# Performance work log

Measured on AMD Instinct MI355X. Metric: run time of the kernel, lower is better.

Reference implementation:

```python
import jax, jax.numpy as jnp
import numpy as np

N = 50000              # total nodes
E = 800000             # random edges (self loops added inside reference, as PyG GATConv does)
FD = 3                 # feature_dim_node
C = 64                 # hidden_channels (= out after heads=1 concat)
OUT = 64               # out_channels of conv2
FC = 512               # fc_hidden_dim
NODES_PER_GRAPH = 5000
NUM_GRAPHS = N // NODES_PER_GRAPH
NEG_SLOPE = 0.2        # PyG GATConv default negative_slope


def _gat(x, W, a_s, a_d, b, src, dst):
    """Single-head PyG GATConv: gather -> leaky_relu -> segment softmax over dst -> scatter-sum."""
    n = x.shape[0]
    h = x @ W                       # [N, C]
    e_s = h @ a_s                   # [N] alpha contribution of source nodes
    e_d = h @ a_d                   # [N] alpha contribution of dest nodes
    e = e_s[src] + e_d[dst]         # [E+N] per-edge logits
    e = jnp.where(e > 0, e, NEG_SLOPE * e)  # leaky_relu
    m = jax.ops.segment_max(e, dst, num_segments=n)
    p = jnp.exp(e - m[dst])
    s = jax.ops.segment_sum(p, dst, num_segments=n)
    alpha = p / s[dst]              # segment softmax over incoming edges of each dst
    out = jax.ops.segment_sum(alpha[:, None] * h[src], dst, num_segments=n)
    return out + b


def setup_inputs() -> dict:
    key = jax.random.key(0)
    ks = jax.random.split(key, 20)
    p = lambda k, shape: (jax.random.normal(k, shape, jnp.float32) * 0.1)
    inp = {
        "x": jax.random.normal(ks[0], (N, FD), jnp.float32),
        "edge_index": jax.random.randint(ks[1], (2, E), 0, N, jnp.int64),
        # conv1: FD -> C
        "W1": p(ks[2], (FD, C)), "as1": p(ks[3], (C,)), "ad1": p(ks[4], (C,)), "b1": p(ks[5], (C,)),
        # 2 hidden convs: C -> C (num_layers - 2 = 2)
        "Wh": p(ks[6], (2, C, C)), "ash": p(ks[7], (2, C)), "adh": p(ks[8], (2, C)), "bh": p(ks[9], (2, C)),
        # conv2: C -> OUT
        "W2": p(ks[10], (C, OUT)), "as2": p(ks[11], (OUT,)), "ad2": p(ks[12], (OUT,)), "b2": p(ks[13], (OUT,)),
        # value head MLP
        "Wv1": p(ks[14], (OUT, FC)), "bv1": p(ks[15], (FC,)),
        "Wv2": p(ks[16], (FC, 1)), "bv2": p(ks[17], (1,)),
    }
    return inp


def reference(x, edge_index, W1, as1, ad1, b1, Wh, ash, adh, bh,
              W2, as2, ad2, b2, Wv1, bv1, Wv2, bv2):
    loops = jnp.arange(N, dtype=edge_index.dtype)
    src = jnp.concatenate([edge_index[0], loops])   # add self loops (PyG default)
    dst = jnp.concatenate([edge_index[1], loops])

    h = jax.nn.relu(_gat(x, W1, as1, ad1, b1, src, dst))
    for i in range(2):  # fixed small layer loop
        h = jax.nn.relu(_gat(h, Wh[i], ash[i], adh[i], bh[i], src, dst))
    h = _gat(h, W2, as2, ad2, b2, src, dst)          # [N, OUT] node embeddings (no relu)

    batch = jnp.arange(N) // NODES_PER_GRAPH          # create_batch_tensor
    pooled = jax.ops.segment_sum(h, batch, num_segments=NUM_GRAPHS) / NODES_PER_GRAPH
    value = jax.nn.relu(pooled @ Wv1 + bv1) @ Wv2 + bv2   # [NUM_GRAPHS, 1]
    return h, pooled, value
```

## Files before the change

kernel.cpp:

```cpp
#include <hip/hip_runtime.h>
#include <hip/hip_fp16.h>
#include <math.h>

#define NN 50000
#define EE 800000
#define TOT_EDGES (EE + NN)
#define FD 3
#define C 64
#define FC 512
#define NODES_PER_GRAPH 5000
#define NUM_GRAPHS 10
#define POOL_CHUNKS 40
#define POOL_NODES_PER_CHUNK 125
#define NEG_SLOPE 0.2f

#define SCAN_BLK 1024
#define SCAN_GRID ((NN + SCAN_BLK - 1) / SCAN_BLK)

#define HC_BLOCKS 1024

#define NPART 8
#define PART_NODES ((NN + NPART - 1) / NPART)
#define CSR_EPT 8
#define CSR_CHUNK (256 * CSR_EPT)
#define CSR_CHUNKS ((TOT_EDGES + CSR_CHUNK - 1) / CSR_CHUNK)


__global__ void k_init_counts(int* counts) {
    int i = blockIdx.x * blockDim.x + threadIdx.x;
    if (i < NN) counts[i] = 0;
}

__global__ void k_count_part(const int* __restrict__ dst, int* __restrict__ counts) {
    int part = blockIdx.x & (NPART - 1);
    int chunk = blockIdx.x >> 3;
    int lo = part * PART_NODES, hi = lo + PART_NODES;
    int base = chunk * CSR_CHUNK + threadIdx.x;
#pragma unroll
    for (int e = 0; e < CSR_EPT; ++e) {
        int i = base + e * 256;
        if (i < TOT_EDGES) {
            int d = (i < EE) ? dst[i] : (i - EE);
            if (d >= lo && d < hi) atomicAdd(&counts[d], 1);
        }
    }
}

__global__ void k_scan1(const int* __restrict__ counts, int* __restrict__ offsets,
                        int* __restrict__ blocksums) {
    int tid = threadIdx.x, blk = blockIdx.x;
    int i = blk * SCAN_BLK + tid;
    int v = (i < NN) ? counts[i] : 0;
    __shared__ int buf[SCAN_BLK];
    buf[tid] = v;
    __syncthreads();
    for (int off = 1; off < SCAN_BLK; off <<= 1) {
        int t = (tid >= off) ? buf[tid - off] : 0;
        __syncthreads();
        buf[tid] += t;
        __syncthreads();
    }
    if (i < NN) offsets[i] = buf[tid] - v;
    if (tid == SCAN_BLK - 1) blocksums[blk] = buf[tid];
}

__global__ void k_scan2(int* __restrict__ blocksums, int* __restrict__ offsets) {
    if (threadIdx.x == 0) {
        int run = 0;
        for (int b = 0; b < SCAN_GRID; ++b) {
            int v = blocksums[b];
            blocksums[b] = run;
            run += v;
        }
        offsets[NN] = run;
    }
}

__global__ void k_scan3(int* __restrict__ offsets, int* __restrict__ cursors,
                        const int* __restrict__ blocksums) {
    int tid = threadIdx.x, blk = blockIdx.x;
    int i = blk * SCAN_BLK + tid;
    if (i < NN) {
        int o = offsets[i] + blocksums[blk];
        offsets[i] = o;
        cursors[i] = o;
    }
}

__global__ void k_scatter_part(const int* __restrict__ src, const int* __restrict__ dst,
                               int* __restrict__ cursors, int* __restrict__ ssrc) {
    int part = blockIdx.x & (NPART - 1);
    int chunk = blockIdx.x >> 3;
    int lo = part * PART_NODES, hi = lo + PART_NODES;
    int base = chunk * CSR_CHUNK + threadIdx.x;
#pragma unroll
    for (int e = 0; e < CSR_EPT; ++e) {
        int i = base + e * 256;
        if (i < TOT_EDGES) {
            int d = (i < EE) ? dst[i] : (i - EE);
            if (d >= lo && d < hi) {
                int s = (i < EE) ? src[i] : d;
                int idx = atomicAdd(&cursors[d], 1);
                ssrc[idx] = s;
            }
        }
    }
}


__global__ void k_hcompute_f3(const float* __restrict__ x,
                              const float* __restrict__ W,
                              const float* __restrict__ a_s, const float* __restrict__ a_d,
                              __half* __restrict__ h, float* __restrict__ es,
                              float* __restrict__ ed, int nwaves_total) {
    int lane = threadIdx.x & 63;
    int wid = (blockIdx.x * blockDim.x + threadIdx.x) >> 6;

    float wcol[FD];
#pragma unroll
    for (int k = 0; k < FD; ++k) wcol[k] = W[k * 64 + lane];
    float asl = a_s[lane], adl = a_d[lane];

    for (int n = wid; n < NN; n += nwaves_total) {
        int nu = __builtin_amdgcn_readfirstlane(n);
        const float* xrow = x + (size_t)nu * FD;
        float acc = 0.f;
#pragma unroll
        for (int k = 0; k < FD; ++k) acc = fmaf(xrow[k], wcol[k], acc);
        h[(size_t)nu * 64 + lane] = __float2half(acc);
        float vs = acc * asl;
        float vd = acc * adl;
        for (int w = 32; w >= 1; w >>= 1) {
            vs += __shfl_xor(vs, w);
            vd += __shfl_xor(vd, w);
        }
        if (lane == 0) { es[nu] = vs; ed[nu] = vd; }
    }
}

__global__ void k_hcompute_h64(const __half* __restrict__ x,
                               const float* __restrict__ W,
                               const float* __restrict__ a_s, const float* __restrict__ a_d,
                               __half* __restrict__ h, float* __restrict__ es,
                               float* __restrict__ ed, int nwaves_total) {
    int lane = threadIdx.x & 63;
    int wid = (blockIdx.x * blockDim.x + threadIdx.x) >> 6;

    float wcol[64];
#pragma unroll
    for (int k = 0; k < 64; ++k) wcol[k] = W[k * 64 + lane];
    float asl = a_s[lane], adl = a_d[lane];

    for (int n = wid; n < NN; n += nwaves_total) {
        int nu = __builtin_amdgcn_readfirstlane(n);
        const __half2* xr = (const __half2*)(x + (size_t)nu * 64);
        float acc = 0.f;
#pragma unroll
        for (int q = 0; q < 32; ++q) {
            float2 f = __half22float2(xr[q]);
            acc = fmaf(f.x, wcol[2 * q], acc);
            acc = fmaf(f.y, wcol[2 * q + 1], acc);
        }
        h[(size_t)nu * 64 + lane] = __float2half(acc);
        float vs = acc * asl;
        float vd = acc * adl;
        for (int w = 32; w >= 1; w >>= 1) {
            vs += __shfl_xor(vs, w);
            vd += __shfl_xor(vd, w);
        }
        if (lane == 0) { es[nu] = vs; ed[nu] = vd; }
    }
}

template<int HIDDEN>
__global__ void k_aggregate(const __half* __restrict__ h,
                            const float* __restrict__ es, const float* __restrict__ ed,
                            const int* __restrict__ offsets, const int* __restrict__ ssrc,
                            const float* __restrict__ bias,
                            __half* __restrict__ outH, float* __restrict__ outF) {
    int gtid = blockIdx.x * blockDim.x + threadIdx.x;
    int n = gtid >> 6;
    int lane = threadIdx.x & 63;
    if (n >= NN) return;
    int beg = offsets[n], end = offsets[n + 1];
    float ednv = ed[n];

    int grp = lane >> 3;
    int c   = lane & 7;
    float s = 0.f;
    float acc[8];
#pragma unroll
    for (int i = 0; i < 8; ++i) acc[i] = 0.f;

    for (int j0 = beg; j0 < end; j0 += 16) {
        int jg0 = j0 + grp;
        int jg1 = j0 + 8 + grp;
        bool v0 = jg0 < end, v1 = jg1 < end;
        int sj0 = v0 ? ssrc[jg0] : 0;
        int sj1 = v1 ? ssrc[jg1] : 0;
        float4 raw0 = *(const float4*)&h[(size_t)sj0 * 64 + c * 8];
        float4 raw1 = *(const float4*)&h[(size_t)sj1 * 64 + c * 8];
        float e0 = es[sj0] + ednv;
        float e1 = es[sj1] + ednv;
        e0 = (e0 > 0.f) ? e0 : NEG_SLOPE * e0;
        e1 = (e1 > 0.f) ? e1 : NEG_SLOPE * e1;
        float p0 = v0 ? __expf(e0) : 0.f;
        float p1 = v1 ? __expf(e1) : 0.f;
        s += p0;
        const __half2* hp0 = (const __half2*)&raw0;
#pragma unroll
        for (int q = 0; q < 4; ++q) {
            float2 f = __half22float2(hp0[q]);
            acc[2 * q]     = fmaf(p0, f.x, acc[2 * q]);
            acc[2 * q + 1] = fmaf(p0, f.y, acc[2 * q + 1]);
        }
        s += p1;
        const __half2* hp1 = (const __half2*)&raw1;
#pragma unroll
        for (int q = 0; q < 4; ++q) {
            float2 f = __half22float2(hp1[q]);
            acc[2 * q]     = fmaf(p1, f.x, acc[2 * q]);
            acc[2 * q + 1] = fmaf(p1, f.y, acc[2 * q + 1]);
        }
    }
#pragma unroll
    for (int w = 8; w <= 32; w <<= 1) {
        s += __shfl_xor(s, w);
#pragma unroll
        for (int i = 0; i < 8; ++i) acc[i] += __shfl_xor(acc[i], w);
    }
    if (grp == 0) {
        float inv_s = 1.0f / s;
        float v[8];
#pragma unroll
        for (int i = 0; i < 8; ++i) {
            v[i] = acc[i] * inv_s + bias[c * 8 + i];
            if (HIDDEN) v[i] = fmaxf(v[i], 0.f);
        }
        if (HIDDEN) {
            __half2 hv[4];
#pragma unroll
            for (int q = 0; q < 4; ++q)
                hv[q] = __floats2half2_rn(v[2 * q], v[2 * q + 1]);
            *(float4*)&outH[(size_t)n * 64 + c * 8] = *(float4*)hv;
        } else {
            *(float4*)&outF[(size_t)n * 64 + c * 8]     = make_float4(v[0], v[1], v[2], v[3]);
            *(float4*)&outF[(size_t)n * 64 + c * 8 + 4] = make_float4(v[4], v[5], v[6], v[7]);
        }
    }
}


__global__ void k_pool1(const float* __restrict__ h, float* __restrict__ partial) {
    int blk = blockIdx.x;
    int g = blk / POOL_CHUNKS, c = blk % POOL_CHUNKS;
    int wave = threadIdx.x >> 6, lane = threadIdx.x & 63;
    int base = g * NODES_PER_GRAPH + c * POOL_NODES_PER_CHUNK;
    float acc = 0.f;
    for (int i = wave; i < POOL_NODES_PER_CHUNK; i += 4)
        acc += h[(size_t)(base + i) * 64 + lane];
    __shared__ float buf[4][64];
    buf[wave][lane] = acc;
    __syncthreads();
    if (wave == 0)
        partial[blk * 64 + lane] = buf[0][lane] + buf[1][lane] + buf[2][lane] + buf[3][lane];
}

__global__ void k_pool2(const float* __restrict__ partial, float* __restrict__ pooled) {
    int g = blockIdx.x;
    int lane = threadIdx.x;
    float acc = 0.f;
    for (int c = 0; c < POOL_CHUNKS; ++c)
        acc += partial[(g * POOL_CHUNKS + c) * 64 + lane];
    pooled[g * 64 + lane] = acc * (1.0f / NODES_PER_GRAPH);
}

__global__ void k_value(const float* __restrict__ pooled,
                        const float* __restrict__ Wv1, const float* __restrict__ bv1,
                        const float* __restrict__ Wv2, const float* __restrict__ bv2,
                        float* __restrict__ value) {
    int g = blockIdx.x;
    int j = threadIdx.x;
    __shared__ float pl[64];
    if (j < 64) pl[j] = pooled[g * 64 + j];
    __syncthreads();
    float acc = bv1[j];
    for (int c = 0; c < 64; ++c) acc += pl[c] * Wv1[c * 512 + j];
    acc = fmaxf(acc, 0.f);
    float t = acc * Wv2[j];
    for (int w = 32; w >= 1; w >>= 1) t += __shfl_xor(t, w);
    __shared__ float red[8];
    int wave = j >> 6, lane = j & 63;
    if (lane == 0) red[wave] = t;
    __syncthreads();
    if (j == 0) {
        float v = 0.f;
        for (int w = 0; w < 8; ++w) v += red[w];
        value[g] = v + bv2[0];
    }
}


extern "C" void kernel_launch(void* const* d_in, const int* in_sizes, int n_in,
                              void* d_out, int out_size, void* d_ws, size_t ws_size,
                              hipStream_t stream) {
    const float* x   = (const float*)d_in[0];
    const int*   ei  = (const int*)d_in[1];
    const float* W1  = (const float*)d_in[2];
    const float* as1 = (const float*)d_in[3];
    const float* ad1 = (const float*)d_in[4];
    const float* b1  = (const float*)d_in[5];
    const float* Wh  = (const float*)d_in[6];
    const float* ash = (const float*)d_in[7];
    const float* adh = (const float*)d_in[8];
    const float* bh  = (const float*)d_in[9];
    const float* W2  = (const float*)d_in[10];
    const float* as2 = (const float*)d_in[11];
    const float* ad2 = (const float*)d_in[12];
    const float* b2  = (const float*)d_in[13];
    const float* Wv1 = (const float*)d_in[14];
    const float* bv1 = (const float*)d_in[15];
    const float* Wv2 = (const float*)d_in[16];
    const float* bv2 = (const float*)d_in[17];

    const int* e_src = ei;
    const int* e_dst = ei + EE;

    char* p = (char*)d_ws;
    auto carve = [&](size_t bytes) {
        char* r = p;
        p += (bytes + 255) & ~(size_t)255;
        return r;
    };
    int*    counts    = (int*)carve(NN * 4);
    int*    offsets   = (int*)carve((NN + 1) * 4);
    int*    cursors   = (int*)carve(NN * 4);
    int*    ssrc      = (int*)carve(TOT_EDGES * 4);
    int*    blocksums = (int*)carve(SCAN_GRID * 4);
    __half* bufH      = (__half*)carve((size_t)NN * 64 * 2);
    __half* bufB16    = (__half*)carve((size_t)NN * 64 * 2);
    float*  es        = (float*)carve(NN * 4);
    float*  ed        = (float*)carve(NN * 4);
    float*  partial   = (float*)carve((size_t)NUM_GRAPHS * POOL_CHUNKS * 64 * 4);

    float* out_h      = (float*)d_out;
    float* out_pooled = out_h + (size_t)NN * 64;
    float* out_value  = out_pooled + NUM_GRAPHS * 64;

    k_init_counts<<<(NN + 255) / 256, 256, 0, stream>>>(counts);
    k_count_part<<<NPART * CSR_CHUNKS, 256, 0, stream>>>(e_dst, counts);
    k_scan1<<<SCAN_GRID, SCAN_BLK, 0, stream>>>(counts, offsets, blocksums);
    k_scan2<<<1, 64, 0, stream>>>(blocksums, offsets);
    k_scan3<<<SCAN_GRID, SCAN_BLK, 0, stream>>>(offsets, cursors, blocksums);
    k_scatter_part<<<NPART * CSR_CHUNKS, 256, 0, stream>>>(e_src, e_dst, cursors, ssrc);

    const int HBLK = (NN + 3) / 4;
    const int HC_WAVES = HC_BLOCKS * 256 / 64;

    k_hcompute_f3<<<HC_BLOCKS, 256, 0, stream>>>(x, W1, as1, ad1, bufH, es, ed, HC_WAVES);
    k_aggregate<1><<<HBLK, 256, 0, stream>>>(bufH, es, ed, offsets, ssrc, b1, bufB16, nullptr);

    for (int i = 0; i < 2; ++i) {
        k_hcompute_h64<<<HC_BLOCKS, 256, 0, stream>>>(bufB16, Wh + i * 64 * 64, ash + i * 64,
                                                      adh + i * 64, bufH, es, ed, HC_WAVES);
        k_aggregate<1><<<HBLK, 256, 0, stream>>>(bufH, es, ed, offsets, ssrc, bh + i * 64,
                                                 bufB16, nullptr);
    }

    k_hcompute_h64<<<HC_BLOCKS, 256, 0, stream>>>(bufB16, W2, as2, ad2, bufH, es, ed, HC_WAVES);
    k_aggregate<0><<<HBLK, 256, 0, stream>>>(bufH, es, ed, offsets, ssrc, b2, nullptr, out_h);

    k_pool1<<<NUM_GRAPHS * POOL_CHUNKS, 256, 0, stream>>>(out_h, partial);
    k_pool2<<<NUM_GRAPHS, 64, 0, stream>>>(partial, out_pooled);
    k_value<<<NUM_GRAPHS, 512, 0, stream>>>(out_pooled, Wv1, bv1, Wv2, bv2, out_value);
}
```

Before: 280.3 us.

## Compute hidden-layer linear transforms with MFMA 16x16x32 f16 instructions

Replaces the per-node scalar FMA dense transform (one wave per node, 64 FMAs per lane) with a matrix-core kernel in which each wave computes a 16-row stripe using mfma_f32_16x16x32_f16. Weights are pre-packed once into fp16 fragment layout by a new small kernel. The attention dot products are reduced with shuffles over the accumulator layout. This cuts ALU work and redundant weight loads in the three 64x64 transforms, at the cost of fp16 weight rounding and one extra launch.

```diff
diff --git a/kernel.cpp b/kernel.cpp
--- a/kernel.cpp
+++ b/kernel.cpp
@@ -19,11 +19,17 @@
 
 #define HC_BLOCKS 1024
 
+#define STRIPES (NN / 16)
+#define MFMA_BLOCKS ((STRIPES + 3) / 4)
+
 #define NPART 8
 #define PART_NODES ((NN + NPART - 1) / NPART)
 #define CSR_EPT 8
 #define CSR_CHUNK (256 * CSR_EPT)
 #define CSR_CHUNKS ((TOT_EDGES + CSR_CHUNK - 1) / CSR_CHUNK)
+
+typedef _Float16 f16x8 __attribute__((ext_vector_type(8)));
+typedef float f32x4 __attribute__((ext_vector_type(4)));
 
 
 __global__ void k_init_counts(int* counts) {
@@ -107,6 +113,20 @@
     }
 }
 
+__global__ void k_wpack(const float* __restrict__ Wh, const float* __restrict__ W2,
+                        __half* __restrict__ wpack) {
+    int tid = blockIdx.x * blockDim.x + threadIdx.x;
+    if (tid >= 3 * 8 * 64) return;
+    int l = tid & 63, f = (tid >> 6) & 7, layer = tid >> 9;
+    const float* W = (layer == 0) ? Wh : (layer == 1) ? (Wh + 4096) : W2;
+    int t = f >> 1, h = f & 1;
+#pragma unroll
+    for (int j = 0; j < 8; ++j) {
+        float w = W[(h * 32 + (l >> 4) * 8 + j) * 64 + (t * 16 + (l & 15))];
+        wpack[(size_t)tid * 8 + j] = __float2half(w);
+    }
+}
+
 
 __global__ void k_hcompute_f3(const float* __restrict__ x,
                               const float* __restrict__ W,
@@ -138,37 +158,61 @@
     }
 }
 
-__global__ void k_hcompute_h64(const __half* __restrict__ x,
-                               const float* __restrict__ W,
-                               const float* __restrict__ a_s, const float* __restrict__ a_d,
-                               __half* __restrict__ h, float* __restrict__ es,
-                               float* __restrict__ ed, int nwaves_total) {
+__global__ void k_hc_mfma(const __half* __restrict__ X,
+                          const __half* __restrict__ wpack,
+                          const float* __restrict__ a_s, const float* __restrict__ a_d,
+                          __half* __restrict__ H, float* __restrict__ es,
+                          float* __restrict__ ed) {
     int lane = threadIdx.x & 63;
-    int wid = (blockIdx.x * blockDim.x + threadIdx.x) >> 6;
-
-    float wcol[64];
-#pragma unroll
-    for (int k = 0; k < 64; ++k) wcol[k] = W[k * 64 + lane];
-    float asl = a_s[lane], adl = a_d[lane];
-
-    for (int n = wid; n < NN; n += nwaves_total) {
-        int nu = __builtin_amdgcn_readfirstlane(n);
-        const __half2* xr = (const __half2*)(x + (size_t)nu * 64);
-        float acc = 0.f;
-#pragma unroll
-        for (int q = 0; q < 32; ++q) {
-            float2 f = __half22float2(xr[q]);
-            acc = fmaf(f.x, wcol[2 * q], acc);
-            acc = fmaf(f.y, wcol[2 * q + 1], acc);
-        }
-        h[(size_t)nu * 64 + lane] = __float2half(acc);
-        float vs = acc * asl;
-        float vd = acc * adl;
-        for (int w = 32; w >= 1; w >>= 1) {
-            vs += __shfl_xor(vs, w);
-            vd += __shfl_xor(vd, w);
-        }
-        if (lane == 0) { es[nu] = vs; ed[nu] = vd; }
+    int stripe = (blockIdx.x * blockDim.x + threadIdx.x) >> 6;
+    if (stripe >= STRIPES) return;
+    int rowbase = stripe * 16;
+    int lr = lane & 15, lg = lane >> 4;
+
+    f16x8 b[8];
+    const float4* wp = (const float4*)wpack;
+#pragma unroll
+    for (int f = 0; f < 8; ++f) {
+        float4 raw = wp[f * 64 + lane];
+        b[f] = *(const f16x8*)&raw;
+    }
+    const __half* xrow = X + (size_t)(rowbase + lr) * 64 + lg * 8;
+    float4 a0raw = *(const float4*)xrow;
+    float4 a1raw = *(const float4*)(xrow + 32);
+    f16x8 a0 = *(const f16x8*)&a0raw;
+    f16x8 a1 = *(const f16x8*)&a1raw;
+
+    float esa[4] = {0.f, 0.f, 0.f, 0.f};
+    float eda[4] = {0.f, 0.f, 0.f, 0.f};
+#pragma unroll
+    for (int t = 0; t < 4; ++t) {
+        f32x4 acc = {0.f, 0.f, 0.f, 0.f};
+        acc = __builtin_amdgcn_mfma_f32_16x16x32_f16(a0, b[t * 2], acc, 0, 0, 0);
+        acc = __builtin_amdgcn_mfma_f32_16x16x32_f16(a1, b[t * 2 + 1], acc, 0, 0, 0);
+        float asv = a_s[t * 16 + lr];
+        float adv = a_d[t * 16 + lr];
+#pragma unroll
+        for (int r = 0; r < 4; ++r) {
+            float v = acc[r];
+            H[(size_t)(rowbase + lg * 4 + r) * 64 + t * 16 + lr] = __float2half(v);
+            esa[r] = fmaf(v, asv, esa[r]);
+            eda[r] = fmaf(v, adv, eda[r]);
+        }
+    }
+#pragma unroll
+    for (int w = 1; w <= 8; w <<= 1) {
+#pragma unroll
+        for (int r = 0; r < 4; ++r) {
+            esa[r] += __shfl_xor(esa[r], w);
+            eda[r] += __shfl_xor(eda[r], w);
+        }
+    }
+    if (lr == 0) {
+#pragma unroll
+        for (int r = 0; r < 4; ++r) {
+            es[rowbase + lg * 4 + r] = esa[r];
+            ed[rowbase + lg * 4 + r] = eda[r];
+        }
     }
 }
 
@@ -337,6 +381,7 @@
     int*    cursors   = (int*)carve(NN * 4);
     int*    ssrc      = (int*)carve(TOT_EDGES * 4);
     int*    blocksums = (int*)carve(SCAN_GRID * 4);
+    __half* wpack     = (__half*)carve(3 * 8 * 64 * 8 * 2);
     __half* bufH      = (__half*)carve((size_t)NN * 64 * 2);
     __half* bufB16    = (__half*)carve((size_t)NN * 64 * 2);
     float*  es        = (float*)carve(NN * 4);
@@ -353,21 +398,25 @@
     k_scan2<<<1, 64, 0, stream>>>(blocksums, offsets);
     k_scan3<<<SCAN_GRID, SCAN_BLK, 0, stream>>>(offsets, cursors, blocksums);
     k_scatter_part<<<NPART * CSR_CHUNKS, 256, 0, stream>>>(e_src, e_dst, cursors, ssrc);
+    k_wpack<<<6, 256, 0, stream>>>(Wh, W2, wpack);
 
     const int HBLK = (NN + 3) / 4;
     const int HC_WAVES = HC_BLOCKS * 256 / 64;
+    const int WPL = 8 * 64 * 8;
 
     k_hcompute_f3<<<HC_BLOCKS, 256, 0, stream>>>(x, W1, as1, ad1, bufH, es, ed, HC_WAVES);
     k_aggregate<1><<<HBLK, 256, 0, stream>>>(bufH, es, ed, offsets, ssrc, b1, bufB16, nullptr);
 
     for (int i = 0; i < 2; ++i) {
-        k_hcompute_h64<<<HC_BLOCKS, 256, 0, stream>>>(bufB16, Wh + i * 64 * 64, ash + i * 64,
-                                                      adh + i * 64, bufH, es, ed, HC_WAVES);
+        k_hc_mfma<<<MFMA_BLOCKS, 256, 0, stream>>>(bufB16, wpack + i * WPL,
+                                                   ash + i * 64, adh + i * 64,
+                                                   bufH, es, ed);
         k_aggregate<1><<<HBLK, 256, 0, stream>>>(bufH, es, ed, offsets, ssrc, bh + i * 64,
                                                  bufB16, nullptr);
     }
 
-    k_hcompute_h64<<<HC_BLOCKS, 256, 0, stream>>>(bufB16, W2, as2, ad2, bufH, es, ed, HC_WAVES);
+    k_hc_mfma<<<MFMA_BLOCKS, 256, 0, stream>>>(bufB16, wpack + 2 * WPL, as2, ad2,
+                                               bufH, es, ed);
     k_aggregate<0><<<HBLK, 256, 0, stream>>>(bufH, es, ed, offsets, ssrc, b2, nullptr, out_h);
 
     k_pool1<<<NUM_GRAPHS * POOL_CHUNKS, 256, 0, stream>>>(out_h, partial);
```

New measurement: 255.9 us. -8.7%, faster.
